# Kernel tuning notes

Hardware: AMD Instinct MI355X
Metric: run time of the kernel (lower is better)

Reference implementation:

```python
import jax, jax.numpy as jnp
import numpy as np

N_NODES = 2048
IN_FEAT = 128
N_HEADS = 4
N_HIDDEN = 16  # out_features // n_heads = 64 // 4
NEG_SLOPE = 0.2


def setup_inputs() -> dict:
    key = jax.random.key(0)
    k1, k2, k3, k4, k5 = jax.random.split(key, 5)
    h = jax.random.normal(k1, (N_NODES, IN_FEAT), dtype=jnp.float32)
    adj_mat = jax.random.randint(k2, (N_NODES, N_NODES, 1), 0, 2, dtype=jnp.int32)
    scale_w = 1.0 / np.sqrt(IN_FEAT)
    W_l = jax.random.normal(k3, (IN_FEAT, N_HEADS * N_HIDDEN), dtype=jnp.float32) * scale_w
    W_r = jax.random.normal(k4, (IN_FEAT, N_HEADS * N_HIDDEN), dtype=jnp.float32) * scale_w
    attn_w = jax.random.normal(k5, (N_HIDDEN,), dtype=jnp.float32) / np.sqrt(N_HIDDEN)
    return {"h": h, "adj_mat": adj_mat, "W_l": W_l, "W_r": W_r, "attn_w": attn_w}


def reference(h, adj_mat, W_l, W_r, attn_w):
    n = h.shape[0]
    g_l = (h @ W_l).reshape(n, N_HEADS, N_HIDDEN)  # source-side proj
    g_r = (h @ W_r).reshape(n, N_HEADS, N_HIDDEN)  # target-side proj
    # g_sum[i, j, h, f] = g_r[i] + g_l[j]  (matches repeat / repeat_interleave in torch)
    g_sum = g_r[:, None, :, :] + g_l[None, :, :, :]  # [N, N, H, F]
    e = jnp.einsum('ijhf,f->ijh', jax.nn.leaky_relu(g_sum, NEG_SLOPE), attn_w)
    e = jnp.where(adj_mat == 0, -jnp.inf, e)
    a = jnp.nan_to_num(jax.nn.softmax(e, axis=1))  # softmax over neighbors j
    attn_res = jnp.einsum('ijh,jhf->ihf', a, g_r)
    return attn_res.reshape(n, N_HEADS * N_HIDDEN)  # is_concat=True
```

## Files before the change

kernel.cpp:

```cpp
#include <hip/hip_runtime.h>
#include <math.h>
#include <stdint.h>

#define NN 2048
#define IF 128
#define NH 4
#define NF 16
#define OF 64
#define JS 4
#define JT 8
#define NPB 16
#define PSTR 17
#define LOG2E 1.44269504f

typedef float f32x2 __attribute__((ext_vector_type(2)));
typedef float f32x4 __attribute__((ext_vector_type(4)));

__device__ __forceinline__ float rfl(float x) {
    return __int_as_float(__builtin_amdgcn_readfirstlane(__float_as_int(x)));
}
__device__ __forceinline__ void gl2lds16(const void* g, void* l) {
    __builtin_amdgcn_global_load_lds((const __attribute__((address_space(1))) void*)g,
                                     (__attribute__((address_space(3))) void*)l, 16, 0, 0);
}
__device__ __forceinline__ void gl2lds4(const void* g, void* l) {
    __builtin_amdgcn_global_load_lds((const __attribute__((address_space(1))) void*)g,
                                     (__attribute__((address_space(3))) void*)l, 4, 0, 0);
}

__global__ __launch_bounds__(256) void pack_kernel(const int* __restrict__ adj,
                                                   uint32_t* __restrict__ bits) {
    const int w = threadIdx.x >> 6, lane = threadIdx.x & 63;
    const int i = blockIdx.x * 4 + w;
    const int* row = adj + (size_t)i * NN;
    uint64_t*  dst = (uint64_t*)bits + (size_t)i * 32;
    #pragma unroll 4
    for (int k = 0; k < 32; ++k) {
        const int v = row[k * 64 + lane];
        const uint64_t msk = __ballot(v != 0);
        if (lane == 0) dst[k] = msk;
    }
}

__global__ __launch_bounds__(256) void proj_kernel(const float* __restrict__ h,
                                                   const float* __restrict__ Wl,
                                                   const float* __restrict__ Wr,
                                                   const float* __restrict__ attn_w,
                                                   float* __restrict__ glt,
                                                   float* __restrict__ grt,
                                                   float* __restrict__ cj6,
                                                   float* __restrict__ cjB,
                                                   float* __restrict__ ai2) {
    const int t    = threadIdx.x;
    const int w    = t >> 6, lane = t & 63;
    const int il   = w >> 1, which = w & 1;
    const int i    = blockIdx.x * 2 + il;

    __shared__ float hs[2][IF];
    hs[t >> 7][t & 127] = h[(blockIdx.x * 2 + (t >> 7)) * IF + (t & 127)];
    __syncthreads();

    const float* W = which ? Wr : Wl;
    float acc = 0.f;
    #pragma unroll
    for (int k = 0; k < IF; ++k)
        acc = fmaf(hs[il][k], W[k * OF + lane], acc);

    float* g = which ? grt : glt;
    g[(lane >> 4) * (NN * NF) + i * NF + (lane & 15)] = acc;

    const float awv = attn_w[lane & 15];
    float v  = acc * awv;
    float vb = fabsf(acc) * fabsf(awv);
    #pragma unroll
    for (int off = 1; off <= 8; off <<= 1) {
        v  += __shfl_xor(v,  off);
        vb += __shfl_xor(vb, off);
    }
    if ((lane & 15) == 0) {
        const int hh = lane >> 4;
        if (which) {
            ai2[hh * NN + i] = 0.4f * LOG2E * vb;
        } else {
            const float c2 = 0.6f * LOG2E * v;
            cj6[hh * NN + i] = c2;
            cjB[hh * NN + i] = fmaf(0.4f * LOG2E, vb, c2);
        }
    }
}

__global__ __launch_bounds__(256) void mh_kernel(const float* __restrict__ cjB,
                                                 float* __restrict__ mh) {
    const int hh = blockIdx.x, t = threadIdx.x;
    float mx = -INFINITY;
    for (int j = t; j < NN; j += 256) mx = fmaxf(mx, cjB[hh * NN + j]);
    #pragma unroll
    for (int off = 32; off; off >>= 1) mx = fmaxf(mx, __shfl_xor(mx, off));
    __shared__ float wmx[4];
    if ((t & 63) == 0) wmx[t >> 6] = mx;
    __syncthreads();
    if (t == 0) mh[hh] = fmaxf(fmaxf(wmx[0], wmx[1]), fmaxf(wmx[2], wmx[3]));
}

__global__ __launch_bounds__(256) __attribute__((amdgpu_waves_per_eu(2, 4)))
void gat_kernel(const float* __restrict__ glt,
                const float* __restrict__ grt,
                const float* __restrict__ cj6,
                const float* __restrict__ ai2,
                const float* __restrict__ mh,
                const uint32_t* __restrict__ bits,
                const float* __restrict__ attn_w,
                float* __restrict__ part) {
    const int t    = threadIdx.x;
    const int wid  = t >> 6, lane = t & 63;
    const int h    = blockIdx.x & 3;
    const int grp  = (blockIdx.x >> 2) & 127;
    const int s    = blockIdx.x >> 9;

    __shared__ __attribute__((aligned(16))) float g_s[2][64 * NF];
    __shared__ __attribute__((aligned(16))) float r_s[2][64 * NF];
    __shared__ uint32_t bits_s[NPB * 16];
    __shared__ float    c_all[JT * 64];
    __shared__ float    red[4][16][NF + 1];

    {
        const int idx = wid * 64 + lane;
        gl2lds4(bits + ((size_t)(grp * 16 + (idx >> 4))) * 64 + s * 16 + (idx & 15),
                (char*)bits_s + (wid * 64) * 4);
    }
    {
        const float* cjh = cj6 + h * NN + s * (JT * 64);
        #pragma unroll
        for (int k = 0; k < 2; ++k)
            gl2lds4(cjh + k * 256 + wid * 64 + lane,
                    (char*)c_all + (k * 256 + wid * 64) * 4);
    }

    float aw_s[NF];
    #pragma unroll
    for (int f = 0; f < NF; ++f) aw_s[f] = rfl(attn_w[f]) * (0.4f * LOG2E);
    const float mh_s = rfl(mh[h]);
    float gi_s[4][NF], cni[4];
    #pragma unroll
    for (int n = 0; n < 4; ++n) {
        const int i_n = grp * 16 + wid * 4 + n;
        #pragma unroll
        for (int f = 0; f < NF; ++f)
            gi_s[n][f] = rfl(grt[h * (NN * NF) + i_n * NF + f]);
        cni[n] = -(rfl(ai2[h * NN + i_n]) + mh_s);
    }

    const float* glh = glt + (size_t)h * NN * NF + (size_t)s * JT * 64 * NF;
    const float* grh = grt + (size_t)h * NN * NF + (size_t)s * JT * 64 * NF;

    const int soff = (wid * 16 + (lane >> 2)) * NF + (((lane & 3) ^ ((lane >> 3) & 3)) << 2);

#define STAGE(tile, nb)                                                   \
    {                                                                     \
        gl2lds16(glh + (size_t)(tile) * 64 * NF + soff, &g_s[nb][wid * 16 * NF]); \
        gl2lds16(grh + (size_t)(tile) * 64 * NF + soff, &r_s[nb][wid * 16 * NF]); \
    }

    float l[4];
    f32x2 acc[4][8];
    #pragma unroll
    for (int n = 0; n < 4; ++n) {
        l[n] = 0.f;
        #pragma unroll
        for (int k = 0; k < 8; ++k) acc[n][k] = (f32x2){0.f, 0.f};
    }

    STAGE(0, 0);
    __syncthreads();

    const int sh = lane & 31;
    #pragma unroll 2
    for (int tt = 0; tt < JT; ++tt) {
        const int buf = tt & 1;
        if (tt + 1 < JT) STAGE(tt + 1, buf ^ 1);

        f32x4 rv[4];
        float ss[4] = {0.f, 0.f, 0.f, 0.f};
        #pragma unroll
        for (int q = 0; q < 4; ++q) {
            const int c = q ^ ((lane >> 1) & 3);
            const f32x4 gv = *(const f32x4*)&g_s[buf][lane * NF + c * 4];
            rv[q] = *(const f32x4*)&r_s[buf][lane * NF + c * 4];
            #pragma unroll
            for (int n = 0; n < 4; ++n) {
                ss[n] = fmaf(fabsf(gv[0] + gi_s[n][q * 4 + 0]), aw_s[q * 4 + 0], ss[n]);
                ss[n] = fmaf(fabsf(gv[1] + gi_s[n][q * 4 + 1]), aw_s[q * 4 + 1], ss[n]);
                ss[n] = fmaf(fabsf(gv[2] + gi_s[n][q * 4 + 2]), aw_s[q * 4 + 2], ss[n]);
                ss[n] = fmaf(fabsf(gv[3] + gi_s[n][q * 4 + 3]), aw_s[q * 4 + 3], ss[n]);
            }
        }
        const float cj = c_all[tt * 64 + lane];

        float p[4];
        #pragma unroll
        for (int n = 0; n < 4; ++n) {
            const uint32_t wb = bits_s[(wid * 4 + n) * 16 + tt * 2 + (lane >> 5)];
            const bool  kk = ((wb >> sh) & 1u) != 0u;
            float e = (ss[n] + cj) + cni[n];
            e = kk ? e : -INFINITY;
            const float pp = __builtin_amdgcn_exp2f(e);
            l[n] += pp;
            p[n] = pp;
        }

        #pragma unroll
        for (int q = 0; q < 4; ++q) {
            const f32x2 lo = {rv[q][0], rv[q][1]};
            const f32x2 hi = {rv[q][2], rv[q][3]};
            #pragma unroll
            for (int n = 0; n < 4; ++n) {
                const f32x2 pp2 = {p[n], p[n]};
                acc[n][q * 2 + 0] = __builtin_elementwise_fma(pp2, lo, acc[n][q * 2 + 0]);
                acc[n][q * 2 + 1] = __builtin_elementwise_fma(pp2, hi, acc[n][q * 2 + 1]);
            }
        }
        __syncthreads();
    }
#undef STAGE

    #pragma unroll
    for (int n = 0; n < 4; ++n) {
        float L = l[n];
        #pragma unroll
        for (int off = 32; off; off >>= 1) L += __shfl_xor(L, off);

        #pragma unroll
        for (int f = 0; f < NF; ++f) {
            float a = acc[n][f >> 1][f & 1];
            a += __shfl_xor(a, 32);
            a += __shfl_xor(a, 16);
            if (lane < 16) red[wid][lane][f] = a;
        }
        const int i_n = grp * 16 + wid * 4 + n;
        float* P = part + ((size_t)s * NH * NN + (size_t)h * NN + i_n) * PSTR;
        if (lane < NF) {
            float a = 0.f;
            #pragma unroll
            for (int r = 0; r < 16; ++r) a += red[wid][r][lane];
            P[lane] = a;
        } else if (lane == 16) P[16] = L;
    }
}

__global__ __launch_bounds__(256) void reduce_kernel(const float* __restrict__ part,
                                                     float* __restrict__ out) {
    const int c  = blockIdx.x * 256 + threadIdx.x;
    const int f  = c & 15;
    const int ih = c >> 4;
    float L = 0.f, a = 0.f;
    #pragma unroll
    for (int ss = 0; ss < JS; ++ss) {
        const float* P = part + ((size_t)ss * NH * NN + ih) * PSTR;
        a += P[f];
        L += P[16];
    }
    const float o = (L > 0.f) ? a / L : 0.f;
    const int i = ih & (NN - 1);
    const int h = ih >> 11;
    out[(size_t)i * OF + h * NF + f] = o;
}

extern "C" void kernel_launch(void* const* d_in, const int* in_sizes, int n_in,
                              void* d_out, int out_size, void* d_ws, size_t ws_size,
                              hipStream_t stream) {
    const float* h      = (const float*)d_in[0];
    const int*   adj    = (const int*)d_in[1];
    const float* W_l    = (const float*)d_in[2];
    const float* W_r    = (const float*)d_in[3];
    const float* attn_w = (const float*)d_in[4];
    float*       out    = (float*)d_out;

    float*    glt  = (float*)d_ws;
    float*    grt  = glt + (size_t)NN * OF;
    float*    cj6  = grt + (size_t)NN * OF;
    float*    cjB  = cj6 + (size_t)NH * NN;
    float*    ai2  = cjB + (size_t)NH * NN;
    float*    mh   = ai2 + (size_t)NH * NN;
    uint32_t* bits = (uint32_t*)(mh + 64);
    float*    prt  = (float*)(bits + (size_t)NN * 64);

    pack_kernel<<<NN / 4, 256, 0, stream>>>(adj, bits);
    proj_kernel<<<NN / 2, 256, 0, stream>>>(h, W_l, W_r, attn_w, glt, grt, cj6, cjB, ai2);
    mh_kernel<<<NH, 256, 0, stream>>>(cjB, mh);
    gat_kernel<<<JS * 128 * NH, 256, 0, stream>>>(glt, grt, cj6, ai2, mh, bits, attn_w, prt);
    reduce_kernel<<<NH * NN * NF / 256, 256, 0, stream>>>(prt, out);
}
```

Baseline: 70.26 us.

## Halve nodes per wave and j-splits, shrink shared memory to raise occupancy

Each wave now handles 2 target nodes instead of 4, with 8 nodes per block and twice as many node groups. The j range is split 2 ways instead of 4, so each block walks 16 tiles. The per-head c values are now streamed per tile into a double buffer instead of preloaded, and the reduction scratch reuses the tile buffer. Register and LDS use drop, so the waves-per-EU hint is raised to 8. In exchange each staged g/r tile is reused by fewer nodes, which doubles the total LDS staging traffic per unit of work.

```diff
diff --git a/kernel.cpp b/kernel.cpp
--- a/kernel.cpp
+++ b/kernel.cpp
@@ -7,11 +7,13 @@
 #define NH 4
 #define NF 16
 #define OF 64
-#define JS 4
-#define JT 8
-#define NPB 16
+#define JS 2
+#define JT 16
+#define NPW 2
+#define NPB 8
 #define PSTR 17
 #define LOG2E 1.44269504f
+
 
 typedef float f32x2 __attribute__((ext_vector_type(2)));
 typedef float f32x4 __attribute__((ext_vector_type(4)));
@@ -102,7 +104,7 @@
     if (t == 0) mh[hh] = fmaxf(fmaxf(wmx[0], wmx[1]), fmaxf(wmx[2], wmx[3]));
 }
 
-__global__ __launch_bounds__(256) __attribute__((amdgpu_waves_per_eu(2, 4)))
+__global__ __launch_bounds__(256) __attribute__((amdgpu_waves_per_eu(2, 8)))
 void gat_kernel(const float* __restrict__ glt,
                 const float* __restrict__ grt,
                 const float* __restrict__ cj6,
@@ -114,36 +116,28 @@
     const int t    = threadIdx.x;
     const int wid  = t >> 6, lane = t & 63;
     const int h    = blockIdx.x & 3;
-    const int grp  = (blockIdx.x >> 2) & 127;
-    const int s    = blockIdx.x >> 9;
-
-    __shared__ __attribute__((aligned(16))) float g_s[2][64 * NF];
-    __shared__ __attribute__((aligned(16))) float r_s[2][64 * NF];
-    __shared__ uint32_t bits_s[NPB * 16];
-    __shared__ float    c_all[JT * 64];
-    __shared__ float    red[4][16][NF + 1];
+    const int grp  = (blockIdx.x >> 2) & 255;
+    const int s    = blockIdx.x >> 10;
+
+    __shared__ __attribute__((aligned(16))) char smem[17920];
+    float*    tile   = (float*)smem;
+    uint32_t* bits_s = (uint32_t*)(smem + 16384);
+    float*    c_s    = (float*)(smem + 17408);
 
     {
         const int idx = wid * 64 + lane;
-        gl2lds4(bits + ((size_t)(grp * 16 + (idx >> 4))) * 64 + s * 16 + (idx & 15),
-                (char*)bits_s + (wid * 64) * 4);
-    }
-    {
-        const float* cjh = cj6 + h * NN + s * (JT * 64);
-        #pragma unroll
-        for (int k = 0; k < 2; ++k)
-            gl2lds4(cjh + k * 256 + wid * 64 + lane,
-                    (char*)c_all + (k * 256 + wid * 64) * 4);
+        gl2lds4(bits + ((size_t)(grp * 8 + (idx >> 5))) * 64 + s * 32 + (idx & 31),
+                smem + 16384 + wid * 256);
     }
 
     float aw_s[NF];
     #pragma unroll
     for (int f = 0; f < NF; ++f) aw_s[f] = rfl(attn_w[f]) * (0.4f * LOG2E);
     const float mh_s = rfl(mh[h]);
-    float gi_s[4][NF], cni[4];
-    #pragma unroll
-    for (int n = 0; n < 4; ++n) {
-        const int i_n = grp * 16 + wid * 4 + n;
+    float gi_s[NPW][NF], cni[NPW];
+    #pragma unroll
+    for (int n = 0; n < NPW; ++n) {
+        const int i_n = grp * NPB + wid * NPW + n;
         #pragma unroll
         for (int f = 0; f < NF; ++f)
             gi_s[n][f] = rfl(grt[h * (NN * NF) + i_n * NF + f]);
@@ -152,19 +146,21 @@
 
     const float* glh = glt + (size_t)h * NN * NF + (size_t)s * JT * 64 * NF;
     const float* grh = grt + (size_t)h * NN * NF + (size_t)s * JT * 64 * NF;
+    const float* cjh = cj6 + h * NN + s * (JT * 64);
 
     const int soff = (wid * 16 + (lane >> 2)) * NF + (((lane & 3) ^ ((lane >> 3) & 3)) << 2);
 
-#define STAGE(tile, nb)                                                   \
-    {                                                                     \
-        gl2lds16(glh + (size_t)(tile) * 64 * NF + soff, &g_s[nb][wid * 16 * NF]); \
-        gl2lds16(grh + (size_t)(tile) * 64 * NF + soff, &r_s[nb][wid * 16 * NF]); \
-    }
-
-    float l[4];
-    f32x2 acc[4][8];
-    #pragma unroll
-    for (int n = 0; n < 4; ++n) {
+#define STAGE(tl, nb)                                                              \
+    {                                                                              \
+        gl2lds16(glh + (size_t)(tl) * (64 * NF) + soff, smem + (nb) * 4096 + wid * 1024);        \
+        gl2lds16(grh + (size_t)(tl) * (64 * NF) + soff, smem + 8192 + (nb) * 4096 + wid * 1024); \
+        if (wid == 0) gl2lds4(cjh + (tl) * 64 + lane, smem + 17408 + (nb) * 256);  \
+    }
+
+    float l[NPW];
+    f32x2 acc[NPW][8];
+    #pragma unroll
+    for (int n = 0; n < NPW; ++n) {
         l[n] = 0.f;
         #pragma unroll
         for (int k = 0; k < 8; ++k) acc[n][k] = (f32x2){0.f, 0.f};
@@ -173,33 +169,32 @@
     STAGE(0, 0);
     __syncthreads();
 
-    const int sh = lane & 31;
+    const int sh   = lane & 31;
+    const int csw  = (lane >> 1) & 3;
     #pragma unroll 2
     for (int tt = 0; tt < JT; ++tt) {
         const int buf = tt & 1;
         if (tt + 1 < JT) STAGE(tt + 1, buf ^ 1);
 
-        f32x4 rv[4];
-        float ss[4] = {0.f, 0.f, 0.f, 0.f};
+        float ss[NPW] = {0.f, 0.f};
         #pragma unroll
         for (int q = 0; q < 4; ++q) {
-            const int c = q ^ ((lane >> 1) & 3);
-            const f32x4 gv = *(const f32x4*)&g_s[buf][lane * NF + c * 4];
-            rv[q] = *(const f32x4*)&r_s[buf][lane * NF + c * 4];
+            const int c = q ^ csw;
+            const f32x4 gv = *(const f32x4*)&tile[buf * 1024 + lane * NF + c * 4];
             #pragma unroll
-            for (int n = 0; n < 4; ++n) {
+            for (int n = 0; n < NPW; ++n) {
                 ss[n] = fmaf(fabsf(gv[0] + gi_s[n][q * 4 + 0]), aw_s[q * 4 + 0], ss[n]);
                 ss[n] = fmaf(fabsf(gv[1] + gi_s[n][q * 4 + 1]), aw_s[q * 4 + 1], ss[n]);
                 ss[n] = fmaf(fabsf(gv[2] + gi_s[n][q * 4 + 2]), aw_s[q * 4 + 2], ss[n]);
                 ss[n] = fmaf(fabsf(gv[3] + gi_s[n][q * 4 + 3]), aw_s[q * 4 + 3], ss[n]);
             }
         }
-        const float cj = c_all[tt * 64 + lane];
-
-        float p[4];
-        #pragma unroll
-        for (int n = 0; n < 4; ++n) {
-            const uint32_t wb = bits_s[(wid * 4 + n) * 16 + tt * 2 + (lane >> 5)];
+        const float cj = c_s[buf * 64 + lane];
+
+        float p[NPW];
+        #pragma unroll
+        for (int n = 0; n < NPW; ++n) {
+            const uint32_t wb = bits_s[(wid * NPW + n) * 32 + tt * 2 + (lane >> 5)];
             const bool  kk = ((wb >> sh) & 1u) != 0u;
             float e = (ss[n] + cj) + cni[n];
             e = kk ? e : -INFINITY;
@@ -210,10 +205,12 @@
 
         #pragma unroll
         for (int q = 0; q < 4; ++q) {
-            const f32x2 lo = {rv[q][0], rv[q][1]};
-            const f32x2 hi = {rv[q][2], rv[q][3]};
+            const int c = q ^ csw;
+            const f32x4 rv = *(const f32x4*)&tile[2048 + buf * 1024 + lane * NF + c * 4];
+            const f32x2 lo = {rv[0], rv[1]};
+            const f32x2 hi = {rv[2], rv[3]};
             #pragma unroll
-            for (int n = 0; n < 4; ++n) {
+            for (int n = 0; n < NPW; ++n) {
                 const f32x2 pp2 = {p[n], p[n]};
                 acc[n][q * 2 + 0] = __builtin_elementwise_fma(pp2, lo, acc[n][q * 2 + 0]);
                 acc[n][q * 2 + 1] = __builtin_elementwise_fma(pp2, hi, acc[n][q * 2 + 1]);
@@ -223,8 +220,9 @@
     }
 #undef STAGE
 
-    #pragma unroll
-    for (int n = 0; n < 4; ++n) {
+    float (*red)[16][PSTR] = (float (*)[16][PSTR])smem;
+    #pragma unroll
+    for (int n = 0; n < NPW; ++n) {
         float L = l[n];
         #pragma unroll
         for (int off = 32; off; off >>= 1) L += __shfl_xor(L, off);
@@ -236,7 +234,7 @@
             a += __shfl_xor(a, 16);
             if (lane < 16) red[wid][lane][f] = a;
         }
-        const int i_n = grp * 16 + wid * 4 + n;
+        const int i_n = grp * NPB + wid * NPW + n;
         float* P = part + ((size_t)s * NH * NN + (size_t)h * NN + i_n) * PSTR;
         if (lane < NF) {
             float a = 0.f;
@@ -287,6 +285,6 @@
     pack_kernel<<<NN / 4, 256, 0, stream>>>(adj, bits);
     proj_kernel<<<NN / 2, 256, 0, stream>>>(h, W_l, W_r, attn_w, glt, grt, cj6, cjB, ai2);
     mh_kernel<<<NH, 256, 0, stream>>>(cjB, mh);
-    gat_kernel<<<JS * 128 * NH, 256, 0, stream>>>(glt, grt, cj6, ai2, mh, bits, attn_w, prt);
+    gat_kernel<<<JS * 256 * NH, 256, 0, stream>>>(glt, grt, cj6, ai2, mh, bits, attn_w, prt);
     reduce_kernel<<<NH * NN * NF / 256, 256, 0, stream>>>(prt, out);
 }
```

Result: faster. 60.74 us (-13.6%).
